# Kernel optimization log

Hardware: AMD Instinct MI355X
Metric: run time of the kernel (lower is better)

## Reference

```python
import jax, jax.numpy as jnp
import numpy as np

EMB_DIM = 1024
HEAD_NUM = 16
HEAD_DIM = EMB_DIM // HEAD_NUM
B, S = 2, 2048


def setup_inputs() -> dict:
    key = jax.random.key(0)
    k_x, k_wqkv, k_bqkv, k_wo, k_bo = jax.random.split(key, 5)
    x = jax.random.normal(k_x, (B, S, EMB_DIM), dtype=jnp.float32)
    # nn.Linear default init scale ~ 1/sqrt(fan_in); exact distribution irrelevant for a reference
    lim = 1.0 / np.sqrt(EMB_DIM)
    W_qkv = jax.random.uniform(k_wqkv, (EMB_DIM, 3 * EMB_DIM), jnp.float32, -lim, lim)
    b_qkv = jax.random.uniform(k_bqkv, (3 * EMB_DIM,), jnp.float32, -lim, lim)
    W_o = jax.random.uniform(k_wo, (EMB_DIM, EMB_DIM), jnp.float32, -lim, lim)
    b_o = jax.random.uniform(k_bo, (EMB_DIM,), jnp.float32, -lim, lim)
    mask = jnp.tril(jnp.ones((S, S), dtype=bool))  # causal mask as in casual_mask(seq_len)
    return {"x": x, "W_qkv": W_qkv, "b_qkv": b_qkv, "W_o": W_o, "b_o": b_o, "mask": mask}


def reference(x, W_qkv, b_qkv, W_o, b_o, mask):
    b, s, e = x.shape
    qkv = x @ W_qkv + b_qkv                      # [b, s, 3e]
    q, k, v = qkv[..., :e], qkv[..., e:2 * e], qkv[..., 2 * e:]
    # [b, s, h, d] -> [b, h, s, d]
    q = q.reshape(b, s, HEAD_NUM, HEAD_DIM).transpose(0, 2, 1, 3)
    k = k.reshape(b, s, HEAD_NUM, HEAD_DIM).transpose(0, 2, 1, 3)
    v = v.reshape(b, s, HEAD_NUM, HEAD_DIM).transpose(0, 2, 1, 3)
    scores = jnp.einsum("bhqd,bhkd->bhqk", q, k) / jnp.sqrt(jnp.float32(HEAD_DIM))
    scores = jnp.where(mask, scores, -jnp.inf)   # masked_fill(~mask, -inf)
    probs = jax.nn.softmax(scores, axis=-1)      # dropout is identity in eval mode
    out = jnp.einsum("bhqk,bhkd->bhqd", probs, v)
    out = out.transpose(0, 2, 1, 3).reshape(b, s, e)
    return out @ W_o + b_o
```

## Files before the change

kernel.cpp:

```cpp
#include <hip/hip_runtime.h>


typedef __attribute__((ext_vector_type(8))) short short8;
typedef __attribute__((ext_vector_type(4))) short short4v;
typedef __attribute__((ext_vector_type(4))) float floatx4;

#define NB 2
#define SEQ 2048
#define EMB 1024
#define NH 16
#define HD 64
#define M_ROWS (NB * SEQ)
#define N_QKV (3 * EMB)
#define SLOT_B 8448

#define GLL(g, l) __builtin_amdgcn_global_load_lds( \
    (const __attribute__((address_space(1))) void*)(g), \
    (__attribute__((address_space(3))) void*)(l), 16, 0, 0)

#if defined(__HIP_DEVICE_COMPILE__)
#define MFMA16K16(A, B, C) __builtin_amdgcn_mfma_f32_16x16x16bf16_1k(A, B, C, 0, 0, 0)
#else
#define MFMA16K16(A, B, C) (C)
#endif

static __device__ __forceinline__ unsigned short f2bf(float f) {
    union { float f; unsigned int u; } v; v.f = f;
    unsigned int r = v.u + 0x7FFFu + ((v.u >> 16) & 1u);
    return (unsigned short)(r >> 16);
}
static __device__ __forceinline__ float bf2f(unsigned short h) {
    union { unsigned int u; float f; } v; v.u = ((unsigned int)h) << 16;
    return v.f;
}

__global__ void prep(const float* __restrict__ x,
                     const float* __restrict__ Wqkv, const float* __restrict__ Wo,
                     unsigned short* __restrict__ x_bf,
                     unsigned short* __restrict__ wqkvT, unsigned short* __restrict__ woT) {
    __shared__ unsigned short tile[32][33];
    int z = blockIdx.z;
    int tx = threadIdx.x, ty = threadIdx.y;
    if (z == 2) {
        int id = ((int)blockIdx.y * 96 + (int)blockIdx.x) * 256 + ty * 32 + tx;
        const int n4 = M_ROWS * EMB / 4;
        for (int i = id; i < n4; i += 96 * 32 * 256) {
            float4 v = ((const float4*)x)[i];
            unsigned long long p = (unsigned long long)f2bf(v.x)
                | ((unsigned long long)f2bf(v.y) << 16)
                | ((unsigned long long)f2bf(v.z) << 32)
                | ((unsigned long long)f2bf(v.w) << 48);
            ((unsigned long long*)x_bf)[i] = p;
        }
        return;
    }
    int C = z ? EMB : N_QKV;
    if ((int)blockIdx.x * 32 >= C) return;
    const float* in = z ? Wo : Wqkv;
    unsigned short* out = z ? woT : wqkvT;
    const int R = EMB;
    int c0 = blockIdx.x * 32, r0 = blockIdx.y * 32;
    #pragma unroll
    for (int j = 0; j < 4; ++j)
        tile[ty + j * 8][tx] = f2bf(in[(size_t)(r0 + ty + j * 8) * C + c0 + tx]);
    __syncthreads();
    #pragma unroll
    for (int j = 0; j < 4; ++j)
        out[(size_t)(c0 + ty + j * 8) * R + r0 + tx] = tile[tx][ty + j * 8];
}

#define CTS 130

__global__ __launch_bounds__(256) void qkv_gemm(
    const unsigned short* __restrict__ A,
    const unsigned short* __restrict__ Bt,
    const float* __restrict__ bias,
    unsigned short* __restrict__ qb, unsigned short* __restrict__ kb,
    unsigned short* __restrict__ vb)
{
    const int K = EMB;
    __shared__ __align__(16) unsigned short smem[128 * CTS];

    int t = threadIdx.x;
    int m0 = blockIdx.y * 128;
    int n0 = blockIdx.x * 128;
    int w = t >> 6, lane = t & 63, quad = lane >> 4, lcol = lane & 15;
    int wr = w >> 1, wc = w & 1;

    floatx4 zero = {0.f, 0.f, 0.f, 0.f};
    floatx4 acc[4][4];
    #pragma unroll
    for (int i = 0; i < 4; ++i)
        #pragma unroll
        for (int j = 0; j < 4; ++j) acc[i][j] = zero;

    const unsigned short* a0 = A  + (size_t)(m0 + (t >> 2)) * K + ((t & 3) << 3);
    const unsigned short* b0 = Bt + (size_t)(n0 + (t >> 2)) * K + ((t & 3) << 3);
    unsigned short* la = &smem[t << 3];

    GLL(a0, la);
    GLL(a0 + 64 * K, la + 2048);
    GLL(b0, la + 4096);
    GLL(b0 + 64 * K, la + 6144);

    for (int k0 = 0; k0 < K; k0 += 32) {
        int cur = (k0 >> 5) & 1, nxt = cur ^ 1;
        __syncthreads();
        if (k0 + 32 < K) {
            GLL(a0 + k0 + 32, la + nxt * 8192);
            GLL(a0 + 64 * K + k0 + 32, la + nxt * 8192 + 2048);
            GLL(b0 + k0 + 32, la + nxt * 8192 + 4096);
            GLL(b0 + 64 * K + k0 + 32, la + nxt * 8192 + 6144);
        }
        const unsigned short* As = &smem[cur * 8192];
        const unsigned short* Bs = As + 4096;
        short8 af[4], bfm[4];
        #pragma unroll
        for (int i = 0; i < 4; ++i)
            af[i] = *(const short8*)(&As[(wr * 64 + i * 16 + lcol) * 32 + quad * 8]);
        #pragma unroll
        for (int j = 0; j < 4; ++j)
            bfm[j] = *(const short8*)(&Bs[(wc * 64 + j * 16 + lcol) * 32 + quad * 8]);
        #pragma unroll
        for (int i = 0; i < 4; ++i)
            #pragma unroll
            for (int j = 0; j < 4; ++j)
                acc[i][j] = __builtin_amdgcn_mfma_f32_16x16x32_bf16(af[i], bfm[j], acc[i][j], 0, 0, 0);
    }

    bool isV = (n0 >= 2 * EMB);
    __syncthreads();
    #pragma unroll
    for (int i = 0; i < 4; ++i) {
        int row0 = wr * 64 + i * 16 + quad * 4;
        #pragma unroll
        for (int j = 0; j < 4; ++j) {
            int col = wc * 64 + j * 16 + lcol;
            float bv = bias[n0 + col];
            #pragma unroll
            for (int r = 0; r < 4; ++r) {
                unsigned short hv = f2bf(acc[i][j][r] + bv);
                if (isV) smem[col * CTS + row0 + r] = hv;
                else     smem[(row0 + r) * CTS + col] = hv;
            }
        }
    }
    __syncthreads();

    int b = m0 >> 11, s0 = m0 & 2047;
    int hbase = (n0 & 1023) >> 6;
    if (!isV) {
        unsigned short* dst = (n0 >= EMB) ? kb : qb;
        #pragma unroll
        for (int it = 0; it < 8; ++it) {
            int job = it * 32 + (t >> 3);
            int tok = job & 127, hh = job >> 7;
            int chunk = t & 7;
            short8 vv = *(const short8*)(&smem[tok * CTS + hh * 64 + chunk * 8]);
            size_t g = ((size_t)((b * NH + hbase + hh) * SEQ + s0 + tok)) * HD + chunk * 8;
            *(short8*)(&dst[g]) = vv;
        }
    } else {
        #pragma unroll
        for (int it = 0; it < 8; ++it) {
            int job = it * 32 + (t >> 3);
            int f = job & 127, half = job >> 7;
            int chunk = (t & 7) + half * 8;
            short8 vv = *(const short8*)(&smem[f * CTS + chunk * 8]);
            int h = hbase + (f >> 6), d = f & 63;
            size_t g = ((size_t)((b * NH + h) * HD + d)) * SEQ + s0 + chunk * 8;
            *(short8*)(&vb[g]) = vv;
        }
    }
}

__global__ __launch_bounds__(256) void attn_partial(
    const unsigned short* __restrict__ Q,
    const unsigned short* __restrict__ Kk,
    const unsigned short* __restrict__ Vt,
    unsigned short* __restrict__ Out,
    unsigned char* __restrict__ Part)
{
    __shared__ __align__(16) unsigned short Ks[2][64 * 64];
    __shared__ __align__(16) unsigned short Vs[2][64 * 64];

    int u = blockIdx.x;
    int bh = blockIdx.y;
    int qt, c;
    if (u < 16) { qt = u; c = 0; }
    else { int v = u - 16; qt = 16 + (v >> 1); c = v & 1; }
    int ktBeg = c << 4;
    int ktEnd = (c == 0 && qt >= 16) ? 16 : (qt + 1);

    int q0 = qt * 64;
    int t = threadIdx.x;
    int w = t >> 6, lane = t & 63, quad = lane >> 4, lcol = lane & 15;
    const size_t hoff = (size_t)bh * SEQ * HD;
    const float SC = 0.18033688011112043f;

    const unsigned short* qp = Q + hoff + (size_t)(q0 + 16 * w + lcol) * HD + quad * 8;
    short8 aq0 = *(const short8*)qp, aq1 = *(const short8*)(qp + 32);

    int srow = t >> 3;
    int ss   = (t & 7) ^ (srow & 7);
    const unsigned short* kgl = Kk + hoff + (size_t)srow * HD + ss * 8;
    const unsigned short* vgl = Vt + hoff + (size_t)srow * SEQ + ss * 8;
    unsigned short* kld = &Ks[0][t * 8];
    unsigned short* vld = &Vs[0][t * 8];

    floatx4 zero = {0.f, 0.f, 0.f, 0.f};
    floatx4 O[4];
    floatx4 lacc = zero;
    #pragma unroll
    for (int d = 0; d < 4; ++d) O[d] = zero;

    short4v ones4;
    #pragma unroll
    for (int j = 0; j < 4; ++j) ones4[j] = (short)0x3F80;

    {
        int k0 = ktBeg * 64;
        GLL(kgl + (size_t)k0 * HD, kld);
        GLL(kgl + (size_t)(k0 + 32) * HD, kld + 2048);
        GLL(vgl + k0, vld);
        GLL(vgl + (size_t)32 * SEQ + k0, vld + 2048);
    }

    int sx0 = (quad ^ (lcol & 7)) << 3;
    int sx1 = sx0 ^ 32;

    for (int kt = ktBeg; kt < ktEnd; ++kt) {
        int cur = kt & 1, nxt = cur ^ 1;
        __syncthreads();
        if (kt + 1 < ktEnd) {
            int k0 = (kt + 1) * 64;
            GLL(kgl + (size_t)k0 * HD, kld + nxt * 4096);
            GLL(kgl + (size_t)(k0 + 32) * HD, kld + nxt * 4096 + 2048);
            GLL(vgl + k0, vld + nxt * 4096);
            GLL(vgl + (size_t)32 * SEQ + k0, vld + nxt * 4096 + 2048);
        }

        const unsigned short* ksr = &Ks[cur][0];
        const unsigned short* vsr = &Vs[cur][0];
        short8 bk0[4], bk1[4];
        #pragma unroll
        for (int tc = 0; tc < 4; ++tc) {
            int rb = (tc * 16 + lcol) << 6;
            bk0[tc] = *(const short8*)(ksr + rb + sx0);
            bk1[tc] = *(const short8*)(ksr + rb + sx1);
        }

        floatx4 sacc[4];
        #pragma unroll
        for (int tc = 0; tc < 4; ++tc) {
            sacc[tc] = __builtin_amdgcn_mfma_f32_16x16x32_bf16(bk0[tc], aq0, zero, 0, 0, 0);
            sacc[tc] = __builtin_amdgcn_mfma_f32_16x16x32_bf16(bk1[tc], aq1, sacc[tc], 0, 0, 0);
        }

        short4v pk[4];
        if (kt == qt) {
            int qrow = q0 + 16 * w + lcol;
            int kbase = kt * 64 + quad * 4;
            #pragma unroll
            for (int tc = 0; tc < 4; ++tc) {
                #pragma unroll
                for (int r = 0; r < 4; ++r) {
                    float p = __builtin_amdgcn_exp2f(sacc[tc][r] * SC);
                    if (kbase + tc * 16 + r > qrow) p = 0.f;
                    pk[tc][r] = (short)f2bf(p);
                }
            }
        } else {
            #pragma unroll
            for (int tc = 0; tc < 4; ++tc) {
                #pragma unroll
                for (int r = 0; r < 4; ++r)
                    pk[tc][r] = (short)f2bf(__builtin_amdgcn_exp2f(sacc[tc][r] * SC));
            }
        }

        #pragma unroll
        for (int td = 0; td < 4; ++td) {
            short4v va[4];
            #pragma unroll
            for (int tc = 0; tc < 4; ++tc) {
                int seg = ((tc << 1) + (quad >> 1)) ^ (lcol & 7);
                va[tc] = *(const short4v*)(vsr + ((td * 16 + lcol) << 6) + (seg << 3) + ((quad & 1) << 2));
            }
            #pragma unroll
            for (int tc = 0; tc < 4; ++tc)
                O[td] = MFMA16K16(va[tc], pk[tc], O[td]);
        }
        #pragma unroll
        for (int tc = 0; tc < 4; ++tc)
            lacc = MFMA16K16(ones4, pk[tc], lacc);
    }

    int qrow = q0 + 16 * w + lcol;
    if (qt < 16) {
        int b = bh >> 4, h = bh & 15;
        float inv = 1.0f / lacc[0];
        size_t obase = ((size_t)b * SEQ + qrow) * EMB + (size_t)h * HD + quad * 4;
        #pragma unroll
        for (int td = 0; td < 4; ++td) {
            short4v ov;
            #pragma unroll
            for (int r = 0; r < 4; ++r) ov[r] = (short)f2bf(O[td][r] * inv);
            *(short4v*)(&Out[obase + td * 16]) = ov;
        }
    } else {
        unsigned char* sp = Part + ((size_t)(bh * 16 + (qt - 16)) * 2 + c) * SLOT_B;
        unsigned short* sO = (unsigned short*)sp;
        float* sL = (float*)(sp + 8192);
        int ql = 16 * w + lcol;
        #pragma unroll
        for (int td = 0; td < 4; ++td) {
            short4v ov;
            #pragma unroll
            for (int r = 0; r < 4; ++r) ov[r] = (short)f2bf(O[td][r]);
            *(short4v*)(&sO[ql * 64 + td * 16 + quad * 4]) = ov;
        }
        if (quad == 0) sL[ql] = lacc[0];
    }
}

__global__ __launch_bounds__(256) void attn_combine(
    const unsigned char* __restrict__ Part, unsigned short* __restrict__ Out)
{
    int qh = blockIdx.x;
    int bh = blockIdx.y;
    int qt = 16 + qh;
    const unsigned char* s0 = Part + ((size_t)(bh * 16 + qh) * 2) * SLOT_B;
    const unsigned char* s1 = s0 + SLOT_B;
    const unsigned short* O0 = (const unsigned short*)s0;
    const unsigned short* O1 = (const unsigned short*)s1;
    const float* L0 = (const float*)(s0 + 8192);
    const float* L1 = (const float*)(s1 + 8192);
    int b = bh >> 4, h = bh & 15;
    size_t obase = ((size_t)b * SEQ + qt * 64) * EMB + (size_t)h * HD;
    int t = threadIdx.x;
    #pragma unroll
    for (int it = 0; it < 16; ++it) {
        int idx = it * 256 + t;
        int row = idx >> 6, col = idx & 63;
        float lv = L0[row] + L1[row];
        float v = (bf2f(O0[idx]) + bf2f(O1[idx])) / lv;
        Out[obase + (size_t)row * EMB + col] = f2bf(v);
    }
}

__global__ __launch_bounds__(256) void oproj_gemm(
    const unsigned short* __restrict__ A,
    const unsigned short* __restrict__ Bt,
    const float* __restrict__ bias,
    float* __restrict__ Cout)
{
    const int K = EMB;
    __shared__ __align__(16) unsigned short smem[2 * 8192];
    int t = threadIdx.x;
    int m0 = blockIdx.y * 128;
    int n0 = blockIdx.x * 128;
    int w = t >> 6, lane = t & 63, quad = lane >> 4, lcol = lane & 15;
    int wr = w >> 1, wc = w & 1;

    floatx4 zero = {0.f, 0.f, 0.f, 0.f};
    floatx4 acc[4][4];
    #pragma unroll
    for (int i = 0; i < 4; ++i)
        #pragma unroll
        for (int j = 0; j < 4; ++j) acc[i][j] = zero;

    const unsigned short* a0 = A  + (size_t)(m0 + (t >> 2)) * K + ((t & 3) << 3);
    const unsigned short* b0 = Bt + (size_t)(n0 + (t >> 2)) * K + ((t & 3) << 3);
    unsigned short* la = &smem[t << 3];

    GLL(a0, la);
    GLL(a0 + 64 * K, la + 2048);
    GLL(b0, la + 4096);
    GLL(b0 + 64 * K, la + 6144);

    for (int k0 = 0; k0 < K; k0 += 32) {
        int cur = (k0 >> 5) & 1, nxt = cur ^ 1;
        __syncthreads();
        if (k0 + 32 < K) {
            GLL(a0 + k0 + 32, la + nxt * 8192);
            GLL(a0 + 64 * K + k0 + 32, la + nxt * 8192 + 2048);
            GLL(b0 + k0 + 32, la + nxt * 8192 + 4096);
            GLL(b0 + 64 * K + k0 + 32, la + nxt * 8192 + 6144);
        }
        const unsigned short* As = &smem[cur * 8192];
        const unsigned short* Bs = As + 4096;
        short8 af[4], bfm[4];
        #pragma unroll
        for (int i = 0; i < 4; ++i)
            af[i] = *(const short8*)(&As[(wr * 64 + i * 16 + lcol) * 32 + quad * 8]);
        #pragma unroll
        for (int j = 0; j < 4; ++j)
            bfm[j] = *(const short8*)(&Bs[(wc * 64 + j * 16 + lcol) * 32 + quad * 8]);
        #pragma unroll
        for (int i = 0; i < 4; ++i)
            #pragma unroll
            for (int j = 0; j < 4; ++j)
                acc[i][j] = __builtin_amdgcn_mfma_f32_16x16x32_bf16(af[i], bfm[j], acc[i][j], 0, 0, 0);
    }

    #pragma unroll
    for (int i = 0; i < 4; ++i) {
        int m = m0 + wr * 64 + i * 16 + quad * 4;
        #pragma unroll
        for (int j = 0; j < 4; ++j) {
            int n = n0 + wc * 64 + j * 16 + lcol;
            float bv = bias[n];
            #pragma unroll
            for (int r = 0; r < 4; ++r)
                Cout[(size_t)(m + r) * EMB + n] = acc[i][j][r] + bv;
        }
    }
}

extern "C" void kernel_launch(void* const* d_in, const int* in_sizes, int n_in,
                              void* d_out, int out_size, void* d_ws, size_t ws_size,
                              hipStream_t stream) {
    (void)in_sizes; (void)n_in; (void)out_size; (void)ws_size;
    char* ws = (char*)d_ws;
    const size_t OFF_X     = 0;
    const size_t OFF_WQKVT = OFF_X     + (size_t)M_ROWS * EMB * 2;
    const size_t OFF_WOT   = OFF_WQKVT + (size_t)N_QKV * EMB * 2;
    const size_t OFF_Q     = OFF_WOT   + (size_t)EMB * EMB * 2;
    const size_t OFF_K     = OFF_Q     + (size_t)M_ROWS * EMB * 2;
    const size_t OFF_V     = OFF_K     + (size_t)M_ROWS * EMB * 2;
    const size_t OFF_ATTN  = OFF_V     + (size_t)M_ROWS * EMB * 2;
    const size_t OFF_PART  = OFF_ATTN  + (size_t)M_ROWS * EMB * 2;

    const float* x    = (const float*)d_in[0];
    const float* Wqkv = (const float*)d_in[1];
    const float* bqkv = (const float*)d_in[2];
    const float* Wo   = (const float*)d_in[3];
    const float* bo   = (const float*)d_in[4];

    unsigned short* x_bf  = (unsigned short*)(ws + OFF_X);
    unsigned short* wqkvT = (unsigned short*)(ws + OFF_WQKVT);
    unsigned short* woT   = (unsigned short*)(ws + OFF_WOT);
    unsigned short* qb    = (unsigned short*)(ws + OFF_Q);
    unsigned short* kb    = (unsigned short*)(ws + OFF_K);
    unsigned short* vb    = (unsigned short*)(ws + OFF_V);
    unsigned short* attn  = (unsigned short*)(ws + OFF_ATTN);
    unsigned char*  part  = (unsigned char*)(ws + OFF_PART);

    prep<<<dim3(96, 32, 3), dim3(32, 8), 0, stream>>>(x, Wqkv, Wo, x_bf, wqkvT, woT);

    qkv_gemm<<<dim3(N_QKV / 128, M_ROWS / 128), 256, 0, stream>>>(x_bf, wqkvT, bqkv, qb, kb, vb);
    attn_partial<<<dim3(48, NB * NH), 256, 0, stream>>>(qb, kb, vb, attn, part);
    attn_combine<<<dim3(16, NB * NH), 256, 0, stream>>>(part, attn);
    oproj_gemm<<<dim3(EMB / 128, M_ROWS / 128), 256, 0, stream>>>(attn, woT, bo, (float*)d_out);
}
```

Measured before the change: 199.0 us.

## Fuse attention into single kernel with 128-row query tiles and balanced scheduling

Replaces the split-K attention (partial kernel plus combine kernel) with one kernel in which each block handles 128 query rows as two 64-row groups that share each loaded K/V tile. Blocks are ordered so long and short causal tiles pair up across the grid, and the partial-output workspace and combine launch are removed. It also switches the bf16 packing to the hardware v_cvt_pk_bf16_f32 instruction. The trade-off is fewer blocks (512 instead of 1536), less parallelism, and more registers per thread.

```diff
diff --git a/kernel.cpp b/kernel.cpp
--- a/kernel.cpp
+++ b/kernel.cpp
@@ -12,7 +12,6 @@
 #define HD 64
 #define M_ROWS (NB * SEQ)
 #define N_QKV (3 * EMB)
-#define SLOT_B 8448
 
 #define GLL(g, l) __builtin_amdgcn_global_load_lds( \
     (const __attribute__((address_space(1))) void*)(g), \
@@ -32,6 +31,22 @@
 static __device__ __forceinline__ float bf2f(unsigned short h) {
     union { unsigned int u; float f; } v; v.u = ((unsigned int)h) << 16;
     return v.f;
+}
+
+static __device__ __forceinline__ unsigned int cvt_pk_bf16(float lo, float hi) {
+#if defined(__HIP_DEVICE_COMPILE__)
+    unsigned int r;
+    asm("v_cvt_pk_bf16_f32 %0, %1, %2" : "=v"(r) : "v"(lo), "v"(hi));
+    return r;
+#else
+    (void)lo; (void)hi; return 0u;
+#endif
+}
+static __device__ __forceinline__ short4v pack4bf(float a, float b, float c, float d) {
+    union { unsigned int u[2]; short4v s; } pu;
+    pu.u[0] = cvt_pk_bf16(a, b);
+    pu.u[1] = cvt_pk_bf16(c, d);
+    return pu.s;
 }
 
 __global__ void prep(const float* __restrict__ x,
@@ -174,32 +189,39 @@
     }
 }
 
-__global__ __launch_bounds__(256) void attn_partial(
+__global__ __launch_bounds__(256) void attn_fused(
     const unsigned short* __restrict__ Q,
     const unsigned short* __restrict__ Kk,
     const unsigned short* __restrict__ Vt,
-    unsigned short* __restrict__ Out,
-    unsigned char* __restrict__ Part)
+    unsigned short* __restrict__ Out)
 {
     __shared__ __align__(16) unsigned short Ks[2][64 * 64];
     __shared__ __align__(16) unsigned short Vs[2][64 * 64];
 
-    int u = blockIdx.x;
-    int bh = blockIdx.y;
-    int qt, c;
-    if (u < 16) { qt = u; c = 0; }
-    else { int v = u - 16; qt = 16 + (v >> 1); c = v & 1; }
-    int ktBeg = c << 4;
-    int ktEnd = (c == 0 && qt >= 16) ? 16 : (qt + 1);
-
-    int q0 = qt * 64;
+    int n = (int)blockIdx.y * 16 + (int)blockIdx.x;
+    int hi = n >> 8;
+    int j = n & 255;
+    int idx = j >> 3;
+    int bh = (j & 7) * 4 + (idx & 3);
+    int qpre = idx >> 2;
+    int qt2 = hi ? (15 - qpre) : qpre;
+
+    int q0 = qt2 * 128;
+    int ktEnd = 2 * (qt2 + 1);
+
     int t = threadIdx.x;
     int w = t >> 6, lane = t & 63, quad = lane >> 4, lcol = lane & 15;
     const size_t hoff = (size_t)bh * SEQ * HD;
     const float SC = 0.18033688011112043f;
 
-    const unsigned short* qp = Q + hoff + (size_t)(q0 + 16 * w + lcol) * HD + quad * 8;
-    short8 aq0 = *(const short8*)qp, aq1 = *(const short8*)(qp + 32);
+    short8 aq[2][2];
+    #pragma unroll
+    for (int g = 0; g < 2; ++g) {
+        const unsigned short* qp = Q + hoff
+            + (size_t)(q0 + g * 64 + 16 * w + lcol) * HD + quad * 8;
+        aq[g][0] = *(const short8*)qp;
+        aq[g][1] = *(const short8*)(qp + 32);
+    }
 
     int srow = t >> 3;
     int ss   = (t & 7) ^ (srow & 7);
@@ -209,27 +231,30 @@
     unsigned short* vld = &Vs[0][t * 8];
 
     floatx4 zero = {0.f, 0.f, 0.f, 0.f};
-    floatx4 O[4];
-    floatx4 lacc = zero;
-    #pragma unroll
-    for (int d = 0; d < 4; ++d) O[d] = zero;
+    floatx4 O[2][4];
+    floatx4 lacc[2];
+    #pragma unroll
+    for (int g = 0; g < 2; ++g) {
+        lacc[g] = zero;
+        #pragma unroll
+        for (int td = 0; td < 4; ++td) O[g][td] = zero;
+    }
 
     short4v ones4;
     #pragma unroll
-    for (int j = 0; j < 4; ++j) ones4[j] = (short)0x3F80;
+    for (int jj = 0; jj < 4; ++jj) ones4[jj] = (short)0x3F80;
 
     {
-        int k0 = ktBeg * 64;
-        GLL(kgl + (size_t)k0 * HD, kld);
-        GLL(kgl + (size_t)(k0 + 32) * HD, kld + 2048);
-        GLL(vgl + k0, vld);
-        GLL(vgl + (size_t)32 * SEQ + k0, vld + 2048);
+        GLL(kgl, kld);
+        GLL(kgl + (size_t)32 * HD, kld + 2048);
+        GLL(vgl, vld);
+        GLL(vgl + (size_t)32 * SEQ, vld + 2048);
     }
 
     int sx0 = (quad ^ (lcol & 7)) << 3;
     int sx1 = sx0 ^ 32;
 
-    for (int kt = ktBeg; kt < ktEnd; ++kt) {
+    for (int kt = 0; kt < ktEnd; ++kt) {
         int cur = kt & 1, nxt = cur ^ 1;
         __syncthreads();
         if (kt + 1 < ktEnd) {
@@ -250,32 +275,41 @@
             bk1[tc] = *(const short8*)(ksr + rb + sx1);
         }
 
-        floatx4 sacc[4];
-        #pragma unroll
-        for (int tc = 0; tc < 4; ++tc) {
-            sacc[tc] = __builtin_amdgcn_mfma_f32_16x16x32_bf16(bk0[tc], aq0, zero, 0, 0, 0);
-            sacc[tc] = __builtin_amdgcn_mfma_f32_16x16x32_bf16(bk1[tc], aq1, sacc[tc], 0, 0, 0);
-        }
-
-        short4v pk[4];
-        if (kt == qt) {
-            int qrow = q0 + 16 * w + lcol;
-            int kbase = kt * 64 + quad * 4;
-            #pragma unroll
-            for (int tc = 0; tc < 4; ++tc) {
+        short4v pk[2][4];
+        bool act[2];
+        #pragma unroll
+        for (int g = 0; g < 2; ++g) {
+            const int gb = q0 + g * 64 + 16 * w;
+            act[g] = (kt * 64 <= gb + 15);
+            if (act[g]) {
+                floatx4 sacc[4];
                 #pragma unroll
-                for (int r = 0; r < 4; ++r) {
-                    float p = __builtin_amdgcn_exp2f(sacc[tc][r] * SC);
-                    if (kbase + tc * 16 + r > qrow) p = 0.f;
-                    pk[tc][r] = (short)f2bf(p);
+                for (int tc = 0; tc < 4; ++tc) {
+                    sacc[tc] = __builtin_amdgcn_mfma_f32_16x16x32_bf16(bk0[tc], aq[g][0], zero, 0, 0, 0);
+                    sacc[tc] = __builtin_amdgcn_mfma_f32_16x16x32_bf16(bk1[tc], aq[g][1], sacc[tc], 0, 0, 0);
                 }
-            }
-        } else {
-            #pragma unroll
-            for (int tc = 0; tc < 4; ++tc) {
-                #pragma unroll
-                for (int r = 0; r < 4; ++r)
-                    pk[tc][r] = (short)f2bf(__builtin_amdgcn_exp2f(sacc[tc][r] * SC));
+                if (kt * 64 + 63 > gb) {
+                    int qrow = gb + lcol;
+                    #pragma unroll
+                    for (int tc = 0; tc < 4; ++tc) {
+                        float p[4];
+                        #pragma unroll
+                        for (int r = 0; r < 4; ++r) {
+                            float e = __builtin_amdgcn_exp2f(sacc[tc][r] * SC);
+                            p[r] = (kt * 64 + tc * 16 + quad * 4 + r > qrow) ? 0.f : e;
+                        }
+                        pk[g][tc] = pack4bf(p[0], p[1], p[2], p[3]);
+                    }
+                } else {
+                    #pragma unroll
+                    for (int tc = 0; tc < 4; ++tc) {
+                        pk[g][tc] = pack4bf(
+                            __builtin_amdgcn_exp2f(sacc[tc][0] * SC),
+                            __builtin_amdgcn_exp2f(sacc[tc][1] * SC),
+                            __builtin_amdgcn_exp2f(sacc[tc][2] * SC),
+                            __builtin_amdgcn_exp2f(sacc[tc][3] * SC));
+                    }
+                }
             }
         }
 
@@ -287,65 +321,40 @@
                 int seg = ((tc << 1) + (quad >> 1)) ^ (lcol & 7);
                 va[tc] = *(const short4v*)(vsr + ((td * 16 + lcol) << 6) + (seg << 3) + ((quad & 1) << 2));
             }
-            #pragma unroll
-            for (int tc = 0; tc < 4; ++tc)
-                O[td] = MFMA16K16(va[tc], pk[tc], O[td]);
-        }
-        #pragma unroll
-        for (int tc = 0; tc < 4; ++tc)
-            lacc = MFMA16K16(ones4, pk[tc], lacc);
-    }
-
-    int qrow = q0 + 16 * w + lcol;
-    if (qt < 16) {
-        int b = bh >> 4, h = bh & 15;
-        float inv = 1.0f / lacc[0];
+            if (act[0]) {
+                #pragma unroll
+                for (int tc = 0; tc < 4; ++tc)
+                    O[0][td] = MFMA16K16(va[tc], pk[0][tc], O[0][td]);
+            }
+            if (act[1]) {
+                #pragma unroll
+                for (int tc = 0; tc < 4; ++tc)
+                    O[1][td] = MFMA16K16(va[tc], pk[1][tc], O[1][td]);
+            }
+        }
+        #pragma unroll
+        for (int g = 0; g < 2; ++g) {
+            if (act[g]) {
+                #pragma unroll
+                for (int tc = 0; tc < 4; ++tc)
+                    lacc[g] = MFMA16K16(ones4, pk[g][tc], lacc[g]);
+            }
+        }
+    }
+
+    int b = bh >> 4, h = bh & 15;
+    #pragma unroll
+    for (int g = 0; g < 2; ++g) {
+        int qrow = q0 + g * 64 + 16 * w + lcol;
+        float inv = 1.0f / lacc[g][0];
         size_t obase = ((size_t)b * SEQ + qrow) * EMB + (size_t)h * HD + quad * 4;
         #pragma unroll
         for (int td = 0; td < 4; ++td) {
             short4v ov;
             #pragma unroll
-            for (int r = 0; r < 4; ++r) ov[r] = (short)f2bf(O[td][r] * inv);
+            for (int r = 0; r < 4; ++r) ov[r] = (short)f2bf(O[g][td][r] * inv);
             *(short4v*)(&Out[obase + td * 16]) = ov;
         }
-    } else {
-        unsigned char* sp = Part + ((size_t)(bh * 16 + (qt - 16)) * 2 + c) * SLOT_B;
-        unsigned short* sO = (unsigned short*)sp;
-        float* sL = (float*)(sp + 8192);
-        int ql = 16 * w + lcol;
-        #pragma unroll
-        for (int td = 0; td < 4; ++td) {
-            short4v ov;
-            #pragma unroll
-            for (int r = 0; r < 4; ++r) ov[r] = (short)f2bf(O[td][r]);
-            *(short4v*)(&sO[ql * 64 + td * 16 + quad * 4]) = ov;
-        }
-        if (quad == 0) sL[ql] = lacc[0];
-    }
-}
-
-__global__ __launch_bounds__(256) void attn_combine(
-    const unsigned char* __restrict__ Part, unsigned short* __restrict__ Out)
-{
-    int qh = blockIdx.x;
-    int bh = blockIdx.y;
-    int qt = 16 + qh;
-    const unsigned char* s0 = Part + ((size_t)(bh * 16 + qh) * 2) * SLOT_B;
-    const unsigned char* s1 = s0 + SLOT_B;
-    const unsigned short* O0 = (const unsigned short*)s0;
-    const unsigned short* O1 = (const unsigned short*)s1;
-    const float* L0 = (const float*)(s0 + 8192);
-    const float* L1 = (const float*)(s1 + 8192);
-    int b = bh >> 4, h = bh & 15;
-    size_t obase = ((size_t)b * SEQ + qt * 64) * EMB + (size_t)h * HD;
-    int t = threadIdx.x;
-    #pragma unroll
-    for (int it = 0; it < 16; ++it) {
-        int idx = it * 256 + t;
-        int row = idx >> 6, col = idx & 63;
-        float lv = L0[row] + L1[row];
-        float v = (bf2f(O0[idx]) + bf2f(O1[idx])) / lv;
-        Out[obase + (size_t)row * EMB + col] = f2bf(v);
     }
 }
 
@@ -430,7 +439,6 @@
     const size_t OFF_K     = OFF_Q     + (size_t)M_ROWS * EMB * 2;
     const size_t OFF_V     = OFF_K     + (size_t)M_ROWS * EMB * 2;
     const size_t OFF_ATTN  = OFF_V     + (size_t)M_ROWS * EMB * 2;
-    const size_t OFF_PART  = OFF_ATTN  + (size_t)M_ROWS * EMB * 2;
 
     const float* x    = (const float*)d_in[0];
     const float* Wqkv = (const float*)d_in[1];
@@ -445,12 +453,10 @@
     unsigned short* kb    = (unsigned short*)(ws + OFF_K);
     unsigned short* vb    = (unsigned short*)(ws + OFF_V);
     unsigned short* attn  = (unsigned short*)(ws + OFF_ATTN);
-    unsigned char*  part  = (unsigned char*)(ws + OFF_PART);
 
     prep<<<dim3(96, 32, 3), dim3(32, 8), 0, stream>>>(x, Wqkv, Wo, x_bf, wqkvT, woT);
 
     qkv_gemm<<<dim3(N_QKV / 128, M_ROWS / 128), 256, 0, stream>>>(x_bf, wqkvT, bqkv, qb, kb, vb);
-    attn_partial<<<dim3(48, NB * NH), 256, 0, stream>>>(qb, kb, vb, attn, part);
-    attn_combine<<<dim3(16, NB * NH), 256, 0, stream>>>(part, attn);
+    attn_fused<<<dim3(16, NB * NH), 256, 0, stream>>>(qb, kb, vb, attn);
     oproj_gemm<<<dim3(EMB / 128, M_ROWS / 128), 256, 0, stream>>>(attn, woT, bo, (float*)d_out);
 }
```

New measurement: 197.8 us. No clear change (-0.6%).
